# Kernel optimization log

Measured on AMD Instinct MI355X. Metric: run time of the kernel, lower is better.

Reference implementation:

```python
import jax, jax.numpy as jnp
import numpy as np

CHUNK = 512  # points per scan step; keeps per-step (B,CHUNK,M) dist tile ~64MB

def _nn_min_sqdist(x, y):
    """Per-point squared distance to nearest neighbor.
    x: (B,N,3), y: (B,M,3) -> (B,N). Chunked over N to avoid a full (B,N,M) matrix.
    """
    B, N, D = x.shape
    y2 = jnp.sum(y * y, axis=-1)  # (B,M)
    nchunks = N // CHUNK
    xc = x.reshape(B, nchunks, CHUNK, D).transpose(1, 0, 2, 3)  # (nchunks,B,C,D)

    def body(carry, xck):  # xck: (B,C,D)
        x2 = jnp.sum(xck * xck, axis=-1)  # (B,C)
        d = x2[:, :, None] + y2[:, None, :] - 2.0 * jnp.einsum('bcd,bmd->bcm', xck, y)
        return carry, jnp.min(d, axis=-1)  # (B,C)

    _, mins = jax.lax.scan(body, None, xc)  # (nchunks,B,C)
    return mins.transpose(1, 0, 2).reshape(B, N)


def setup_inputs() -> dict:
    key = jax.random.key(0)
    k1, k2 = jax.random.split(key)
    pred = jax.random.normal(k1, (4, 8192, 3), dtype=jnp.float32)
    gt = jax.random.normal(k2, (4, 8192, 3), dtype=jnp.float32)
    return {"pred": pred, "gt": gt}


def reference(pred, gt):
    beta, gamma, delta = 1.0, 1.0, 0.0  # ChamferLoss defaults; threshold=None, percentage=1.0
    N = pred.shape[1]
    pred2gt = _nn_min_sqdist(pred, gt)  # (B,N)
    gt2pred = _nn_min_sqdist(gt, pred)  # (B,M)
    loss = (jnp.mean(pred2gt, axis=-1)
            + jnp.mean(gt2pred, axis=-1) * (delta * N + gamma)
            + jnp.max(pred2gt, axis=-1) * beta)
    return jnp.mean(loss)
```

## Files before the change

### kernel.cpp

```cpp
#include <hip/hip_runtime.h>


typedef short  s16x8  __attribute__((ext_vector_type(8)));
typedef float  f32x16 __attribute__((ext_vector_type(16)));

#define BATCH 4
#define NPTS  8192
#define TPB   256
#define YS    4
#define YTILES (NPTS / 32)
#define YTS   (YTILES / YS)
#define XPB   256
#define NXC   (NPTS / XPB)

__device__ __forceinline__ unsigned int bft(float f) { return __float_as_uint(f) >> 16; }
__device__ __forceinline__ float bfv(unsigned int s) { return __uint_as_float(s << 16); }

__global__ __launch_bounds__(TPB)
void yprep(const float* __restrict__ pred, const float* __restrict__ gt,
           uint4* __restrict__ bfrag) {
    const int gid = blockIdx.x * TPB + threadIdx.x;
    const int arr = gid >> 15;
    const int rem = gid & 32767;
    const int yi  = rem & (NPTS - 1);
    const float* y = (arr ? gt : pred) + (size_t)rem * 3;
    const float a0 = y[0], a1 = y[1], a2 = y[2];
    const unsigned int yh0 = bft(a0), yh1 = bft(a1), yh2 = bft(a2);
    const float l0 = a0 - bfv(yh0), l1 = a1 - bfv(yh1), l2 = a2 - bfv(yh2);
    const unsigned int nh0 = bft(-2.f * bfv(yh0));
    const unsigned int nh1 = bft(-2.f * bfv(yh1));
    const unsigned int nh2 = bft(-2.f * bfv(yh2));
    const unsigned int nl0 = bft(-2.f * l0), nl1 = bft(-2.f * l1), nl2 = bft(-2.f * l2);
    const float y2 = a0 * a0 + a1 * a1 + a2 * a2;
    const unsigned int q2h = bft(y2);
    const unsigned int q2l = bft(y2 - bfv(q2h));
    uint4 w0, w1;
    w0.x = nh0 | (nh1 << 16);
    w0.y = nh2 | (nl0 << 16);
    w0.z = nl1 | (nl2 << 16);
    w0.w = nh0 | (nh1 << 16);
    w1.x = nh2 | (q2h << 16);
    w1.y = q2l;
    w1.z = 0u; w1.w = 0u;
    const size_t base = ((size_t)(gid >> 13) * YTILES + (yi >> 5)) * 64;
    bfrag[base + (yi & 31)]      = w0;
    bfrag[base + 32 + (yi & 31)] = w1;
}

__global__ __launch_bounds__(TPB, 4)
void nn_mfma(const float* __restrict__ pred, const float* __restrict__ gt,
             const uint4* __restrict__ bfrag, unsigned int* __restrict__ pmin) {
    const int xc = blockIdx.x, sl = blockIdx.y, bd = blockIdx.z;
    const int b = bd >> 1, dir = bd & 1;
    const float* xp = (dir ? gt : pred) + (size_t)b * NPTS * 3;
    const int yarr = dir ? 0 : 1;
    const uint4* bfb = bfrag + (size_t)(yarr * BATCH + b) * YTILES * 64;

    const int t = threadIdx.x;
    const int w = t >> 6, l = t & 63;
    const int m32 = l & 31, hh = l >> 5;
    const int xbase = xc * XPB + w * 64;

    s16x8 af[2];
    float x2j[2];
    #pragma unroll
    for (int j = 0; j < 2; ++j) {
        const int xi = xbase + j * 32 + m32;
        const float c0 = xp[xi * 3], c1 = xp[xi * 3 + 1], c2 = xp[xi * 3 + 2];
        x2j[j] = c0 * c0 + c1 * c1 + c2 * c2;
        const unsigned int xh0 = bft(c0), xh1 = bft(c1), xh2 = bft(c2);
        const unsigned int xl0 = bft(c0 - bfv(xh0));
        const unsigned int xl1 = bft(c1 - bfv(xh1));
        const unsigned int xl2 = bft(c2 - bfv(xh2));
        s16x8 a;
        a[0] = (short)(hh ? xl2 : xh0);
        a[1] = (short)(hh ? 0x3F80u : xh1);
        a[2] = (short)(hh ? 0x3F80u : xh2);
        a[3] = (short)(hh ? 0u : xh0);
        a[4] = (short)(hh ? 0u : xh1);
        a[5] = (short)(hh ? 0u : xh2);
        a[6] = (short)(hh ? 0u : xl0);
        a[7] = (short)(hh ? 0u : xl1);
        af[j] = a;
    }

    f32x16 zero, mn0, mn1;
    #pragma unroll
    for (int r = 0; r < 16; ++r) { zero[r] = 0.f; mn0[r] = 3.4e38f; mn1[r] = 3.4e38f; }

    const uint4* bp = bfb + (size_t)(sl * YTS) * 64 + l;
    for (int t32 = 0; t32 < YTS; t32 += 2) {
        const s16x8 bf0 = __builtin_bit_cast(s16x8, bp[0]);
        const s16x8 bf1 = __builtin_bit_cast(s16x8, bp[64]);
        bp += 128;
        const f32x16 e00 = __builtin_amdgcn_mfma_f32_32x32x16_bf16(af[0], bf0, zero, 0, 0, 0);
        const f32x16 e01 = __builtin_amdgcn_mfma_f32_32x32x16_bf16(af[0], bf1, zero, 0, 0, 0);
        mn0 = __builtin_elementwise_min(mn0, __builtin_elementwise_min(e00, e01));
        const f32x16 e10 = __builtin_amdgcn_mfma_f32_32x32x16_bf16(af[1], bf0, zero, 0, 0, 0);
        const f32x16 e11 = __builtin_amdgcn_mfma_f32_32x32x16_bf16(af[1], bf1, zero, 0, 0, 0);
        mn1 = __builtin_elementwise_min(mn1, __builtin_elementwise_min(e10, e11));
    }

    #pragma unroll
    for (int off = 16; off; off >>= 1) {
        #pragma unroll
        for (int r = 0; r < 16; ++r) {
            mn0[r] = fminf(mn0[r], __shfl_xor(mn0[r], off, 64));
            mn1[r] = fminf(mn1[r], __shfl_xor(mn1[r], off, 64));
        }
    }

    const int r = l & 15;
    const int row = (r & 3) + 8 * (r >> 2) + 4 * hh;
    float v0 = mn0[0], v1 = mn1[0];
    #pragma unroll
    for (int rr = 1; rr < 16; ++rr) {
        v0 = (r == rr) ? mn0[rr] : v0;
        v1 = (r == rr) ? mn1[rr] : v1;
    }
    const float x20 = __shfl(x2j[0], row, 64);
    const float x21 = __shfl(x2j[1], row, 64);
    const bool g1 = (l & 31) >= 16;
    const float d = fmaxf((g1 ? v1 : v0) + (g1 ? x21 : x20), 0.f);
    const int xpt = xbase + (g1 ? 32 : 0) + row;
    atomicMin(&pmin[(size_t)bd * NPTS + xpt], __float_as_uint(d));
}

__global__ __launch_bounds__(1024)
void reduce_all(const unsigned int* __restrict__ pmin, float* __restrict__ out) {
    const int t  = threadIdx.x;
    const int bd = t >> 7;
    const int l  = t & 127;
    const unsigned int* base = pmin + (size_t)bd * NPTS;
    float sum = 0.f, mx = -1.f;
    #pragma unroll
    for (int i = 0; i < NPTS / 128; ++i) {
        const float f = __uint_as_float(base[i * 128 + l]);
        sum += f;
        mx = fmaxf(mx, f);
    }
    #pragma unroll
    for (int off = 32; off; off >>= 1) {
        sum += __shfl_down(sum, off, 64);
        mx = fmaxf(mx, __shfl_down(mx, off, 64));
    }
    __shared__ float ss[16], sm[16];
    if ((t & 63) == 0) { ss[t >> 6] = sum; sm[t >> 6] = mx; }
    __syncthreads();
    if (t == 0) {
        float acc = 0.f;
        #pragma unroll
        for (int d = 0; d < 8; ++d) {
            const float S = ss[2 * d] + ss[2 * d + 1];
            const float M = fmaxf(sm[2 * d], sm[2 * d + 1]);
            acc += S * (1.f / NPTS) + ((d & 1) ? 0.f : M);
        }
        out[0] = acc * (1.f / BATCH);
    }
}

extern "C" void kernel_launch(void* const* d_in, const int* in_sizes, int n_in,
                              void* d_out, int out_size, void* d_ws, size_t ws_size,
                              hipStream_t stream) {
    const float* pred = (const float*)d_in[0];
    const float* gt   = (const float*)d_in[1];

    unsigned int* pmin = (unsigned int*)d_ws;
    uint4* bfrag = (uint4*)((char*)d_ws + (size_t)2 * BATCH * NPTS * 4);

    hipMemsetAsync(pmin, 0xFF, (size_t)2 * BATCH * NPTS * 4, stream);

    yprep<<<dim3(2 * BATCH * NPTS / TPB), TPB, 0, stream>>>(pred, gt, bfrag);
    dim3 g1(NXC, YS, 2 * BATCH);
    nn_mfma<<<g1, TPB, 0, stream>>>(pred, gt, bfrag, pmin);
    reduce_all<<<dim3(1), 1024, 0, stream>>>(pmin, (float*)d_out);
}
```

Before: 85.94 us.

## Fuse memset into prep kernel, reduce in last block, prefetch B fragments

Moves the pmin initialisation and the done-counter reset into the yprep kernel, which removes the separate memset. The final reduction now runs in the last nn_mfma block to finish, detected through an atomic counter, so the separate reduce_all launch goes away. The inner MFMA loop also software-prefetches the next pair of B fragments before using the current ones. The cost is that the tail reduction runs on 256 threads in a single block, and correctness now depends on the fence and atomic ordering.

```diff
diff --git a/kernel.cpp b/kernel.cpp
--- a/kernel.cpp
+++ b/kernel.cpp
@@ -12,14 +12,18 @@
 #define YTS   (YTILES / YS)
 #define XPB   256
 #define NXC   (NPTS / XPB)
+#define NBLK  (NXC * YS * 2 * BATCH)
 
 __device__ __forceinline__ unsigned int bft(float f) { return __float_as_uint(f) >> 16; }
 __device__ __forceinline__ float bfv(unsigned int s) { return __uint_as_float(s << 16); }
 
 __global__ __launch_bounds__(TPB)
 void yprep(const float* __restrict__ pred, const float* __restrict__ gt,
-           uint4* __restrict__ bfrag) {
+           uint4* __restrict__ bfrag, unsigned int* __restrict__ pmin,
+           unsigned int* __restrict__ done) {
     const int gid = blockIdx.x * TPB + threadIdx.x;
+    pmin[gid] = 0xFFFFFFFFu;
+    if (gid == 0) *done = 0u;
     const int arr = gid >> 15;
     const int rem = gid & 32767;
     const int yi  = rem & (NPTS - 1);
@@ -49,7 +53,8 @@
 
 __global__ __launch_bounds__(TPB, 4)
 void nn_mfma(const float* __restrict__ pred, const float* __restrict__ gt,
-             const uint4* __restrict__ bfrag, unsigned int* __restrict__ pmin) {
+             const uint4* __restrict__ bfrag, unsigned int* __restrict__ pmin,
+             unsigned int* __restrict__ done, float* __restrict__ out) {
     const int xc = blockIdx.x, sl = blockIdx.y, bd = blockIdx.z;
     const int b = bd >> 1, dir = bd & 1;
     const float* xp = (dir ? gt : pred) + (size_t)b * NPTS * 3;
@@ -89,10 +94,22 @@
     for (int r = 0; r < 16; ++r) { zero[r] = 0.f; mn0[r] = 3.4e38f; mn1[r] = 3.4e38f; }
 
     const uint4* bp = bfb + (size_t)(sl * YTS) * 64 + l;
-    for (int t32 = 0; t32 < YTS; t32 += 2) {
-        const s16x8 bf0 = __builtin_bit_cast(s16x8, bp[0]);
-        const s16x8 bf1 = __builtin_bit_cast(s16x8, bp[64]);
-        bp += 128;
+    uint4 c0 = bp[0], c1 = bp[64]; bp += 128;
+    for (int it = 0; it < YTS / 2 - 1; ++it) {
+        const uint4 n0 = bp[0], n1 = bp[64]; bp += 128;
+        const s16x8 bf0 = __builtin_bit_cast(s16x8, c0);
+        const s16x8 bf1 = __builtin_bit_cast(s16x8, c1);
+        const f32x16 e00 = __builtin_amdgcn_mfma_f32_32x32x16_bf16(af[0], bf0, zero, 0, 0, 0);
+        const f32x16 e01 = __builtin_amdgcn_mfma_f32_32x32x16_bf16(af[0], bf1, zero, 0, 0, 0);
+        mn0 = __builtin_elementwise_min(mn0, __builtin_elementwise_min(e00, e01));
+        const f32x16 e10 = __builtin_amdgcn_mfma_f32_32x32x16_bf16(af[1], bf0, zero, 0, 0, 0);
+        const f32x16 e11 = __builtin_amdgcn_mfma_f32_32x32x16_bf16(af[1], bf1, zero, 0, 0, 0);
+        mn1 = __builtin_elementwise_min(mn1, __builtin_elementwise_min(e10, e11));
+        c0 = n0; c1 = n1;
+    }
+    {
+        const s16x8 bf0 = __builtin_bit_cast(s16x8, c0);
+        const s16x8 bf1 = __builtin_bit_cast(s16x8, c1);
         const f32x16 e00 = __builtin_amdgcn_mfma_f32_32x32x16_bf16(af[0], bf0, zero, 0, 0, 0);
         const f32x16 e01 = __builtin_amdgcn_mfma_f32_32x32x16_bf16(af[0], bf1, zero, 0, 0, 0);
         mn0 = __builtin_elementwise_min(mn0, __builtin_elementwise_min(e00, e01));
@@ -124,37 +141,42 @@
     const float d = fmaxf((g1 ? v1 : v0) + (g1 ? x21 : x20), 0.f);
     const int xpt = xbase + (g1 ? 32 : 0) + row;
     atomicMin(&pmin[(size_t)bd * NPTS + xpt], __float_as_uint(d));
-}
 
-__global__ __launch_bounds__(1024)
-void reduce_all(const unsigned int* __restrict__ pmin, float* __restrict__ out) {
-    const int t  = threadIdx.x;
-    const int bd = t >> 7;
-    const int l  = t & 127;
-    const unsigned int* base = pmin + (size_t)bd * NPTS;
+    __shared__ int lastflag;
+    __syncthreads();
+    if (t == 0) {
+        __threadfence();
+        const unsigned int old = atomicAdd(done, 1u);
+        lastflag = (old == NBLK - 1);
+        __threadfence();
+    }
+    __syncthreads();
+    if (!lastflag) return;
+
+    const int gbd = t >> 5, l32 = t & 31;
+    const unsigned int* base = pmin + (size_t)gbd * NPTS;
     float sum = 0.f, mx = -1.f;
-    #pragma unroll
-    for (int i = 0; i < NPTS / 128; ++i) {
-        const float f = __uint_as_float(base[i * 128 + l]);
+    for (int i = 0; i < NPTS / 32; ++i) {
+        const unsigned int u = __hip_atomic_load(&base[i * 32 + l32],
+                                                 __ATOMIC_RELAXED,
+                                                 __HIP_MEMORY_SCOPE_AGENT);
+        const float f = __uint_as_float(u);
         sum += f;
         mx = fmaxf(mx, f);
     }
     #pragma unroll
-    for (int off = 32; off; off >>= 1) {
-        sum += __shfl_down(sum, off, 64);
-        mx = fmaxf(mx, __shfl_down(mx, off, 64));
+    for (int off = 16; off; off >>= 1) {
+        sum += __shfl_down(sum, off, 32);
+        mx = fmaxf(mx, __shfl_down(mx, off, 32));
     }
-    __shared__ float ss[16], sm[16];
-    if ((t & 63) == 0) { ss[t >> 6] = sum; sm[t >> 6] = mx; }
+    __shared__ float ss[8], sm[8];
+    if (l32 == 0) { ss[gbd] = sum; sm[gbd] = mx; }
     __syncthreads();
     if (t == 0) {
         float acc = 0.f;
         #pragma unroll
-        for (int d = 0; d < 8; ++d) {
-            const float S = ss[2 * d] + ss[2 * d + 1];
-            const float M = fmaxf(sm[2 * d], sm[2 * d + 1]);
-            acc += S * (1.f / NPTS) + ((d & 1) ? 0.f : M);
-        }
+        for (int d2 = 0; d2 < 8; d2 += 2)
+            acc += ss[d2] * (1.f / NPTS) + ss[d2 + 1] * (1.f / NPTS) + sm[d2];
         out[0] = acc * (1.f / BATCH);
     }
 }
@@ -167,11 +189,10 @@
 
     unsigned int* pmin = (unsigned int*)d_ws;
     uint4* bfrag = (uint4*)((char*)d_ws + (size_t)2 * BATCH * NPTS * 4);
+    unsigned int* done = (unsigned int*)((char*)d_ws + (size_t)2 * BATCH * NPTS * 4
+                                         + (size_t)2 * BATCH * YTILES * 64 * 16);
 
-    hipMemsetAsync(pmin, 0xFF, (size_t)2 * BATCH * NPTS * 4, stream);
-
-    yprep<<<dim3(2 * BATCH * NPTS / TPB), TPB, 0, stream>>>(pred, gt, bfrag);
+    yprep<<<dim3(2 * BATCH * NPTS / TPB), TPB, 0, stream>>>(pred, gt, bfrag, pmin, done);
     dim3 g1(NXC, YS, 2 * BATCH);
-    nn_mfma<<<g1, TPB, 0, stream>>>(pred, gt, bfrag, pmin);
-    reduce_all<<<dim3(1), 1024, 0, stream>>>(pmin, (float*)d_out);
+    nn_mfma<<<g1, TPB, 0, stream>>>(pred, gt, bfrag, pmin, done, (float*)d_out);
 }
```

Result: slower. 117.1 us (+36.2%).

## Stage Y fragments in LDS via global_load_lds and fold memset into prep

Applied to the files above, without the earlier changes.

The MFMA kernel previously had each of the four waves load the same Y fragments straight from global memory. It now stages a phase of 32 tiles into shared memory cooperatively with direct global-to-LDS loads, separated by barriers, and every wave reads those tiles from LDS. This is meant to cut redundant global or L2 traffic by four. In exchange it adds two barriers per phase and no double buffering, so load latency is exposed. Separately, the memset launch is removed and pmin is initialized inside yprep, saving one launch.

```diff
diff --git a/kernel.cpp b/kernel.cpp
--- a/kernel.cpp
+++ b/kernel.cpp
@@ -10,16 +10,24 @@
 #define YS    4
 #define YTILES (NPTS / 32)
 #define YTS   (YTILES / YS)
+#define PHT   32
 #define XPB   256
 #define NXC   (NPTS / XPB)
 
 __device__ __forceinline__ unsigned int bft(float f) { return __float_as_uint(f) >> 16; }
 __device__ __forceinline__ float bfv(unsigned int s) { return __uint_as_float(s << 16); }
 
+__device__ __forceinline__ void gl_lds16(const uint4* g, uint4* s) {
+    __builtin_amdgcn_global_load_lds(
+        (const __attribute__((address_space(1))) void*)g,
+        (__attribute__((address_space(3))) void*)s, 16, 0, 0);
+}
+
 __global__ __launch_bounds__(TPB)
 void yprep(const float* __restrict__ pred, const float* __restrict__ gt,
-           uint4* __restrict__ bfrag) {
+           uint4* __restrict__ bfrag, unsigned int* __restrict__ pmin) {
     const int gid = blockIdx.x * TPB + threadIdx.x;
+    pmin[gid] = 0xFFFFFFFFu;
     const int arr = gid >> 15;
     const int rem = gid & 32767;
     const int yi  = rem & (NPTS - 1);
@@ -54,7 +62,10 @@
     const int b = bd >> 1, dir = bd & 1;
     const float* xp = (dir ? gt : pred) + (size_t)b * NPTS * 3;
     const int yarr = dir ? 0 : 1;
-    const uint4* bfb = bfrag + (size_t)(yarr * BATCH + b) * YTILES * 64;
+    const uint4* bfb = bfrag + (size_t)(yarr * BATCH + b) * YTILES * 64
+                       + (size_t)(sl * YTS) * 64;
+
+    __shared__ uint4 ystage[PHT * 64];
 
     const int t = threadIdx.x;
     const int w = t >> 6, l = t & 63;
@@ -88,17 +99,27 @@
     #pragma unroll
     for (int r = 0; r < 16; ++r) { zero[r] = 0.f; mn0[r] = 3.4e38f; mn1[r] = 3.4e38f; }
 
-    const uint4* bp = bfb + (size_t)(sl * YTS) * 64 + l;
-    for (int t32 = 0; t32 < YTS; t32 += 2) {
-        const s16x8 bf0 = __builtin_bit_cast(s16x8, bp[0]);
-        const s16x8 bf1 = __builtin_bit_cast(s16x8, bp[64]);
-        bp += 128;
-        const f32x16 e00 = __builtin_amdgcn_mfma_f32_32x32x16_bf16(af[0], bf0, zero, 0, 0, 0);
-        const f32x16 e01 = __builtin_amdgcn_mfma_f32_32x32x16_bf16(af[0], bf1, zero, 0, 0, 0);
-        mn0 = __builtin_elementwise_min(mn0, __builtin_elementwise_min(e00, e01));
-        const f32x16 e10 = __builtin_amdgcn_mfma_f32_32x32x16_bf16(af[1], bf0, zero, 0, 0, 0);
-        const f32x16 e11 = __builtin_amdgcn_mfma_f32_32x32x16_bf16(af[1], bf1, zero, 0, 0, 0);
-        mn1 = __builtin_elementwise_min(mn1, __builtin_elementwise_min(e10, e11));
+    const s16x8* sy = (const s16x8*)ystage;
+    for (int ph = 0; ph < YTS / PHT; ++ph) {
+        #pragma unroll
+        for (int i = 0; i < PHT / 4; ++i) {
+            const int tt = w * (PHT / 4) + i;
+            gl_lds16(bfb + (size_t)(ph * PHT + tt) * 64 + l, ystage + tt * 64);
+        }
+        __syncthreads();
+
+        #pragma unroll 4
+        for (int tt = 0; tt < PHT; tt += 2) {
+            const s16x8 bf0 = sy[tt * 64 + l];
+            const s16x8 bf1 = sy[(tt + 1) * 64 + l];
+            const f32x16 e00 = __builtin_amdgcn_mfma_f32_32x32x16_bf16(af[0], bf0, zero, 0, 0, 0);
+            const f32x16 e01 = __builtin_amdgcn_mfma_f32_32x32x16_bf16(af[0], bf1, zero, 0, 0, 0);
+            mn0 = __builtin_elementwise_min(mn0, __builtin_elementwise_min(e00, e01));
+            const f32x16 e10 = __builtin_amdgcn_mfma_f32_32x32x16_bf16(af[1], bf0, zero, 0, 0, 0);
+            const f32x16 e11 = __builtin_amdgcn_mfma_f32_32x32x16_bf16(af[1], bf1, zero, 0, 0, 0);
+            mn1 = __builtin_elementwise_min(mn1, __builtin_elementwise_min(e10, e11));
+        }
+        __syncthreads();
     }
 
     #pragma unroll
@@ -168,9 +189,7 @@
     unsigned int* pmin = (unsigned int*)d_ws;
     uint4* bfrag = (uint4*)((char*)d_ws + (size_t)2 * BATCH * NPTS * 4);
 
-    hipMemsetAsync(pmin, 0xFF, (size_t)2 * BATCH * NPTS * 4, stream);
-
-    yprep<<<dim3(2 * BATCH * NPTS / TPB), TPB, 0, stream>>>(pred, gt, bfrag);
+    yprep<<<dim3(2 * BATCH * NPTS / TPB), TPB, 0, stream>>>(pred, gt, bfrag, pmin);
     dim3 g1(NXC, YS, 2 * BATCH);
     nn_mfma<<<g1, TPB, 0, stream>>>(pred, gt, bfrag, pmin);
     reduce_all<<<dim3(1), 1024, 0, stream>>>(pmin, (float*)d_out);
```

Result: slower. 100.6 us (+17.1%).
